# Kernel optimization log

Hardware: AMD Instinct MI355X
Metric: run time of the kernel (lower is better)

The kernel has to match this reference:

```python
import jax, jax.numpy as jnp
import numpy as np
from jax import lax

B, C, H, W = 8, 64, 256, 256
LENGTH = 9
REDUCTION = 8
HIDDEN = max(8, C // REDUCTION)


def _conv(x, w, b, pad):
    # x: [B,Cin,H,W], w: [Cout,Cin,kh,kw]
    y = lax.conv_general_dilated(x, w, (1, 1), [(pad, pad), (pad, pad)],
                                 dimension_numbers=('NCHW', 'OIHW', 'NCHW'))
    return y + b[None, :, None, None]


def _bilinear(img, cy, cx):
    # img: [B,C,H,W]; cy,cx: [B,H,W] float coords already clipped to [0, size-1]
    # Matches F.grid_sample(mode='bilinear', padding_mode='border', align_corners=True)
    Hh, Ww = img.shape[2], img.shape[3]
    y0 = jnp.floor(cy)
    x0 = jnp.floor(cx)
    wy = (cy - y0)[:, None]  # [B,1,H,W]
    wx = (cx - x0)[:, None]
    y0i = y0.astype(jnp.int32)
    x0i = x0.astype(jnp.int32)
    y1i = jnp.minimum(y0i + 1, Hh - 1)
    x1i = jnp.minimum(x0i + 1, Ww - 1)

    def g(im, iy, ix):
        return im[:, iy, ix]  # [C,H,W]

    gather = jax.vmap(g)
    v00 = gather(img, y0i, x0i)
    v01 = gather(img, y0i, x1i)
    v10 = gather(img, y1i, x0i)
    v11 = gather(img, y1i, x1i)
    return (v00 * (1 - wy) * (1 - wx) + v01 * (1 - wy) * wx
            + v10 * wy * (1 - wx) + v11 * wy * wx)


def _oriented_pool(x, vx, vy, length):
    # x: [B,C,H,W]; vx,vy: [B,1,H,W] direction fields
    _, _, Hh, Ww = x.shape
    yy = jnp.arange(Hh, dtype=x.dtype)[None, :, None]  # [1,H,1]
    xx = jnp.arange(Ww, dtype=x.dtype)[None, None, :]  # [1,1,W]
    half = length // 2
    offsets = jnp.arange(-half, half + 1, dtype=x.dtype)
    vx2 = vx[:, 0]  # [B,H,W]
    vy2 = vy[:, 0]

    def step(acc, t):
        cy = jnp.clip(yy + t * vy2, 0.0, Hh - 1)
        cx = jnp.clip(xx + t * vx2, 0.0, Ww - 1)
        return acc + _bilinear(x, cy, cx), None

    acc, _ = lax.scan(step, jnp.zeros_like(x), offsets)
    return acc / length


def setup_inputs() -> dict:
    key = jax.random.key(0)
    ks = jax.random.split(key, 5)

    def he(k, shape, fan_in):
        return jax.random.normal(k, shape, jnp.float32) * np.float32(1.0 / np.sqrt(fan_in))

    return {
        'x': jax.random.normal(ks[0], (B, C, H, W), jnp.float32),
        'w3': he(ks[1], (HIDDEN, C, 3, 3), C * 9),
        'b3': jnp.zeros((HIDDEN,), jnp.float32),
        'w1': he(ks[2], (1, HIDDEN, 1, 1), HIDDEN),
        'b1': jnp.zeros((1,), jnp.float32),
        'wr': he(ks[3], (HIDDEN, 2 * C, 1, 1), 2 * C),
        'br': jnp.zeros((HIDDEN,), jnp.float32),
        'we': he(ks[4], (2 * C, HIDDEN, 1, 1), HIDDEN),
        'be': jnp.zeros((2 * C,), jnp.float32),
    }


def reference(x, w3, b3, w1, b1, wr, br, we, be):
    theta = jnp.pi * jax.nn.sigmoid(_conv(jax.nn.relu(_conv(x, w3, b3, 1)), w1, b1, 0))  # [B,1,H,W]
    cos_t = jnp.cos(theta)
    sin_t = jnp.sin(theta)
    tan_feat = _oriented_pool(x, cos_t, sin_t, LENGTH)
    nor_feat = _oriented_pool(x, -sin_t, cos_t, LENGTH)
    context = jnp.concatenate([tan_feat, nor_feat], axis=1)  # [B,2C,H,W]
    w = jax.nn.sigmoid(_conv(jax.nn.relu(_conv(context, wr, br, 0)), we, be, 0))  # [B,2C,H,W]
    alpha_tan, alpha_norm = jnp.split(w, 2, axis=1)
    return (alpha_tan + alpha_norm) * x
```

## Files before the change

kernel.cpp:

```cpp
#include <hip/hip_runtime.h>
#include <math.h>

#define Bb 8
#define Cc 64
#define Hh 256
#define Ww 256
#define HID 8
#define PLANE (Hh*Ww)

#define T2H 6
#define T2W 66
#define T2P 67
#define T2N (T2H*T2W)

__global__ __launch_bounds__(256, 4) void theta_kernel(
    const float* __restrict__ x, const float* __restrict__ w3,
    const float* __restrict__ b3, const float* __restrict__ w1,
    const float* __restrict__ b1, float* __restrict__ cosout,
    float* __restrict__ sinout)
{
    __shared__ float2 tile[T2H * T2P];
    const int tid = threadIdx.x;
    const int tx = tid & 63;
    const int ty = tid >> 6;
    const int xx = blockIdx.x * 64 + tx;
    const int yy = blockIdx.y * 4 + ty;
    const int b  = blockIdx.z;
    const int row0 = blockIdx.y * 4 - 1;
    const int col0 = blockIdx.x * 64 - 1;

    const float* xb = x + (size_t)b * Cc * PLANE;

    int goff[2], loff[2];
    bool intile[2], inimg[2];
    #pragma unroll
    for (int k = 0; k < 2; k++) {
        const int i  = tid + k * 256;
        const int r  = i / T2W;
        const int cc = i - r * T2W;
        const int gy = row0 + r;
        const int gx = col0 + cc;
        intile[k] = (i < T2N);
        inimg[k]  = intile[k] && gy >= 0 && gy < Hh && gx >= 0 && gx < Ww;
        goff[k] = inimg[k] ? (gy * Ww + gx) : 0;
        loff[k] = r * T2P + cc;
    }

    float acc[HID];
    #pragma unroll
    for (int h = 0; h < HID; h++) acc[h] = 0.f;

    float rvx[2] = {0.f, 0.f}, rvy[2] = {0.f, 0.f};
    #pragma unroll
    for (int k = 0; k < 2; k++) if (inimg[k]) {
        rvx[k] = xb[goff[k]];
        rvy[k] = xb[goff[k] + PLANE];
    }

    const int lbase = (ty + 1) * T2P + (tx + 1);

    for (int cp = 0; cp < Cc / 2; cp++) {
        __syncthreads();
        #pragma unroll
        for (int k = 0; k < 2; k++)
            if (intile[k]) tile[loff[k]] = make_float2(rvx[k], rvy[k]);
        if (cp + 1 < Cc / 2) {
            const float* xn = xb + (size_t)(2 * (cp + 1)) * PLANE;
            #pragma unroll
            for (int k = 0; k < 2; k++) if (inimg[k]) {
                rvx[k] = xn[goff[k]];
                rvy[k] = xn[goff[k] + PLANE];
            }
        }
        __syncthreads();

        float2 v[9];
        #pragma unroll
        for (int dy = 0; dy < 3; dy++)
            #pragma unroll
            for (int dx = 0; dx < 3; dx++)
                v[dy * 3 + dx] = tile[lbase + (dy - 1) * T2P + (dx - 1)];

        #pragma unroll
        for (int h = 0; h < HID; h++) {
            const float* wk = w3 + (size_t)(h * Cc + 2 * cp) * 9;
            float a = acc[h];
            #pragma unroll
            for (int k = 0; k < 9; k++) a = fmaf(wk[k],     v[k].x, a);
            #pragma unroll
            for (int k = 0; k < 9; k++) a = fmaf(wk[9 + k], v[k].y, a);
            acc[h] = a;
        }
    }

    float z = b1[0];
    #pragma unroll
    for (int h = 0; h < HID; h++) {
        float hr = acc[h] + b3[h];
        hr = hr > 0.f ? hr : 0.f;
        z = fmaf(w1[h], hr, z);
    }
    const float theta = 3.14159265358979f / (1.f + __expf(-z));
    float s, co;
    __sincosf(theta, &s, &co);
    const int p = b * PLANE + yy * Ww + xx;
    cosout[p] = co;
    sinout[p] = s;
}

#define TPH 13
#define TPW 74
#define TPP 75
#define TPN (TPH*TPW)

__global__ __launch_bounds__(256, 3) void pool_kernel(
    const float* __restrict__ x,
    const float* __restrict__ cosb, const float* __restrict__ sinb,
    const float* __restrict__ wr, const float* __restrict__ br,
    const float* __restrict__ we, const float* __restrict__ be,
    float* __restrict__ out)
{
    __shared__ float2 tile[TPH * TPP];
    const int tid = threadIdx.x;
    const int tx = tid & 63;
    const int ty = tid >> 6;
    const int xx = blockIdx.x * 64 + tx;
    const int yy = blockIdx.y * 4 + ty;
    const int b  = blockIdx.z;
    const int p  = b * PLANE + yy * Ww + xx;
    const int row0 = blockIdx.y * 4 - 4;
    const int col0 = blockIdx.x * 64 - 4;

    const float vx = cosb[p];
    const float vy = sinb[p];

    int   off[16];
    float fwy[16], fwx[16];
    #pragma unroll
    for (int s = 0; s < 9; s++) {
        if (s == 4) continue;
        const int j = (s < 4) ? s : s - 1;
        const float t = (float)(s - 4);
        float cy = fminf(fmaxf((float)yy + t * vy, 0.f), (float)(Hh - 1));
        float cx = fminf(fmaxf((float)xx + t * vx, 0.f), (float)(Ww - 1));
        int y0 = min((int)cy, Hh - 2);
        int x0 = min((int)cx, Ww - 2);
        off[j] = (y0 - row0) * TPP + (x0 - col0);
        fwy[j] = cy - (float)y0;
        fwx[j] = cx - (float)x0;
        float cy2 = fminf(fmaxf((float)yy + t * vx, 0.f), (float)(Hh - 1));
        float cx2 = fminf(fmaxf((float)xx - t * vy, 0.f), (float)(Ww - 1));
        int y02 = min((int)cy2, Hh - 2);
        int x02 = min((int)cx2, Ww - 2);
        off[8 + j] = (y02 - row0) * TPP + (x02 - col0);
        fwy[8 + j] = cy2 - (float)y02;
        fwx[8 + j] = cx2 - (float)x02;
    }
    const int lcen = (ty + 4) * TPP + (tx + 4);

    int goff[4], loff[4];
    #pragma unroll
    for (int k = 0; k < 4; k++) {
        int i = tid + k * 256;
        i = (i < TPN) ? i : (TPN - 1);
        const int r  = i / TPW;
        const int cc = i - r * TPW;
        const int gy = min(max(row0 + r, 0), Hh - 1);
        const int gx = min(max(col0 + cc, 0), Ww - 1);
        goff[k] = gy * Ww + gx;
        loff[k] = r * TPP + cc;
    }

    float hid[HID];
    #pragma unroll
    for (int h = 0; h < HID; h++) hid[h] = br[h];

    const float* xb = x + (size_t)b * Cc * PLANE;

    float rvx[4], rvy[4];
    #pragma unroll
    for (int k = 0; k < 4; k++) {
        rvx[k] = xb[goff[k]];
        rvy[k] = xb[goff[k] + PLANE];
    }

    for (int cp = 0; cp < Cc / 2; cp++) {
        __syncthreads();
        #pragma unroll
        for (int k = 0; k < 4; k++)
            tile[loff[k]] = make_float2(rvx[k], rvy[k]);
        if (cp + 1 < Cc / 2) {
            const float* xn = xb + (size_t)(2 * (cp + 1)) * PLANE;
            #pragma unroll
            for (int k = 0; k < 4; k++) {
                rvx[k] = xn[goff[k]];
                rvy[k] = xn[goff[k] + PLANE];
            }
        }
        __syncthreads();

        const float2 cent = tile[lcen];
        float tacc0 = cent.x, tacc1 = cent.y;
        float nacc0 = cent.x, nacc1 = cent.y;
        #pragma unroll
        for (int s = 0; s < 16; s++) {
            const int o = off[s];
            const float2 a00 = tile[o];
            const float2 a01 = tile[o + 1];
            const float2 a10 = tile[o + TPP];
            const float2 a11 = tile[o + TPP + 1];
            const float wx_ = fwx[s], wy_ = fwy[s];
            const float t0  = a00.x + wx_ * (a01.x - a00.x);
            const float b0  = a10.x + wx_ * (a11.x - a10.x);
            const float v0  = t0 + wy_ * (b0 - t0);
            const float t1  = a00.y + wx_ * (a01.y - a00.y);
            const float b1v = a10.y + wx_ * (a11.y - a10.y);
            const float v1  = t1 + wy_ * (b1v - t1);
            if (s < 8) { tacc0 += v0; tacc1 += v1; }
            else       { nacc0 += v0; nacc1 += v1; }
        }
        tacc0 *= (1.f / 9.f); tacc1 *= (1.f / 9.f);
        nacc0 *= (1.f / 9.f); nacc1 *= (1.f / 9.f);
        const int c = 2 * cp;
        #pragma unroll
        for (int h = 0; h < HID; h++) {
            float a = hid[h];
            a = fmaf(wr[h * 128 + c],          tacc0, a);
            a = fmaf(wr[h * 128 + 64 + c],     nacc0, a);
            a = fmaf(wr[h * 128 + c + 1],      tacc1, a);
            a = fmaf(wr[h * 128 + 64 + c + 1], nacc1, a);
            hid[h] = a;
        }
    }

    #pragma unroll
    for (int h = 0; h < HID; h++) hid[h] = fmaxf(hid[h], 0.f);

    const int pix = yy * Ww + xx;
    for (int c = 0; c < Cc; c++) {
        float z1 = be[c];
        float z2 = be[c + 64];
        #pragma unroll
        for (int h = 0; h < HID; h++) {
            z1 = fmaf(we[c * 8 + h],        hid[h], z1);
            z2 = fmaf(we[(c + 64) * 8 + h], hid[h], z2);
        }
        const float a1 = 1.f / (1.f + __expf(-z1));
        const float a2 = 1.f / (1.f + __expf(-z2));
        const float xv = xb[c * PLANE + pix];
        out[(size_t)(b * Cc + c) * PLANE + pix] = (a1 + a2) * xv;
    }
}

extern "C" void kernel_launch(void* const* d_in, const int* in_sizes, int n_in,
                              void* d_out, int out_size, void* d_ws, size_t ws_size,
                              hipStream_t stream) {
    const float* x  = (const float*)d_in[0];
    const float* w3 = (const float*)d_in[1];
    const float* b3 = (const float*)d_in[2];
    const float* w1 = (const float*)d_in[3];
    const float* b1 = (const float*)d_in[4];
    const float* wr = (const float*)d_in[5];
    const float* br = (const float*)d_in[6];
    const float* we = (const float*)d_in[7];
    const float* be = (const float*)d_in[8];
    float* out = (float*)d_out;

    float* cosb = (float*)d_ws;
    float* sinb = cosb + (size_t)Bb * PLANE;

    dim3 grid(Ww / 64, Hh / 4, Bb);
    dim3 block(256);
    theta_kernel<<<grid, block, 0, stream>>>(x, w3, b3, w1, b1, cosb, sinb);
    pool_kernel<<<grid, block, 0, stream>>>(x, cosb, sinb, wr, br, we, be, out);
}
```

Before: 572.1 us.

## Stage more channels per LDS tile pass in theta and pool kernels

The theta kernel now stages 8 channels per iteration in two float4 shared tiles instead of 2 channels in a float2 tile. The pool kernel stages 4 channels per iteration in a float4 tile. Both changes cut the number of barrier-separated iterations and give wider LDS reads, while each bilinear offset and weight now serves more channels. Empty inline asm pins the offsets and weights in VGPRs so they are not rematerialized. The cost is higher register and LDS use (the pool tile doubles and the theta tiles quadruple), which may lower occupancy under the existing launch bounds.

After: 530.6 us. 7.3% less time.

```diff
diff --git a/kernel.cpp b/kernel.cpp
--- a/kernel.cpp
+++ b/kernel.cpp
@@ -8,6 +8,8 @@
 #define HID 8
 #define PLANE (Hh*Ww)
 
+typedef float fvec4 __attribute__((ext_vector_type(4)));
+
 #define T2H 6
 #define T2W 66
 #define T2P 67
@@ -19,7 +21,8 @@
     const float* __restrict__ b1, float* __restrict__ cosout,
     float* __restrict__ sinout)
 {
-    __shared__ float2 tile[T2H * T2P];
+    __shared__ fvec4 tileA[T2H * T2P];
+    __shared__ fvec4 tileB[T2H * T2P];
     const int tid = threadIdx.x;
     const int tx = tid & 63;
     const int ty = tid >> 6;
@@ -50,45 +53,60 @@
     #pragma unroll
     for (int h = 0; h < HID; h++) acc[h] = 0.f;
 
-    float rvx[2] = {0.f, 0.f}, rvy[2] = {0.f, 0.f};
+    float rv[2][8];
+    #pragma unroll
+    for (int k = 0; k < 2; k++)
+        #pragma unroll
+        for (int q = 0; q < 8; q++) rv[k][q] = 0.f;
     #pragma unroll
     for (int k = 0; k < 2; k++) if (inimg[k]) {
-        rvx[k] = xb[goff[k]];
-        rvy[k] = xb[goff[k] + PLANE];
+        #pragma unroll
+        for (int q = 0; q < 8; q++) rv[k][q] = xb[goff[k] + (size_t)q * PLANE];
     }
 
     const int lbase = (ty + 1) * T2P + (tx + 1);
 
-    for (int cp = 0; cp < Cc / 2; cp++) {
+    for (int st = 0; st < Cc / 8; st++) {
         __syncthreads();
         #pragma unroll
-        for (int k = 0; k < 2; k++)
-            if (intile[k]) tile[loff[k]] = make_float2(rvx[k], rvy[k]);
-        if (cp + 1 < Cc / 2) {
-            const float* xn = xb + (size_t)(2 * (cp + 1)) * PLANE;
+        for (int k = 0; k < 2; k++) if (intile[k]) {
+            tileA[loff[k]] = (fvec4){rv[k][0], rv[k][1], rv[k][2], rv[k][3]};
+            tileB[loff[k]] = (fvec4){rv[k][4], rv[k][5], rv[k][6], rv[k][7]};
+        }
+        if (st + 1 < Cc / 8) {
+            const float* xn = xb + (size_t)(st + 1) * 8 * PLANE;
             #pragma unroll
             for (int k = 0; k < 2; k++) if (inimg[k]) {
-                rvx[k] = xn[goff[k]];
-                rvy[k] = xn[goff[k] + PLANE];
+                #pragma unroll
+                for (int q = 0; q < 8; q++)
+                    rv[k][q] = xn[goff[k] + (size_t)q * PLANE];
             }
         }
         __syncthreads();
 
-        float2 v[9];
+        fvec4 va[9], vb[9];
         #pragma unroll
         for (int dy = 0; dy < 3; dy++)
             #pragma unroll
-            for (int dx = 0; dx < 3; dx++)
-                v[dy * 3 + dx] = tile[lbase + (dy - 1) * T2P + (dx - 1)];
+            for (int dx = 0; dx < 3; dx++) {
+                va[dy * 3 + dx] = tileA[lbase + (dy - 1) * T2P + (dx - 1)];
+                vb[dy * 3 + dx] = tileB[lbase + (dy - 1) * T2P + (dx - 1)];
+            }
 
         #pragma unroll
         for (int h = 0; h < HID; h++) {
-            const float* wk = w3 + (size_t)(h * Cc + 2 * cp) * 9;
+            const float* wk = w3 + (size_t)(h * Cc + st * 8) * 9;
             float a = acc[h];
             #pragma unroll
-            for (int k = 0; k < 9; k++) a = fmaf(wk[k],     v[k].x, a);
-            #pragma unroll
-            for (int k = 0; k < 9; k++) a = fmaf(wk[9 + k], v[k].y, a);
+            for (int c = 0; c < 4; c++)
+                #pragma unroll
+                for (int k = 0; k < 9; k++)
+                    a = fmaf(wk[c * 9 + k], va[k][c], a);
+            #pragma unroll
+            for (int c = 0; c < 4; c++)
+                #pragma unroll
+                for (int k = 0; k < 9; k++)
+                    a = fmaf(wk[(4 + c) * 9 + k], vb[k][c], a);
             acc[h] = a;
         }
     }
@@ -120,7 +138,7 @@
     const float* __restrict__ we, const float* __restrict__ be,
     float* __restrict__ out)
 {
-    __shared__ float2 tile[TPH * TPP];
+    __shared__ fvec4 tile[TPH * TPP];
     const int tid = threadIdx.x;
     const int tx = tid & 63;
     const int ty = tid >> 6;
@@ -156,6 +174,10 @@
         fwy[8 + j] = cy2 - (float)y02;
         fwx[8 + j] = cx2 - (float)x02;
     }
+    #pragma unroll
+    for (int s = 0; s < 16; s++)
+        asm volatile("" : "+v"(off[s]), "+v"(fwx[s]), "+v"(fwy[s]));
+
     const int lcen = (ty + 4) * TPP + (tx + 4);
 
     int goff[4], loff[4];
@@ -170,6 +192,9 @@
         goff[k] = gy * Ww + gx;
         loff[k] = r * TPP + cc;
     }
+    #pragma unroll
+    for (int k = 0; k < 4; k++)
+        asm volatile("" : "+v"(goff[k]), "+v"(loff[k]));
 
     float hid[HID];
     #pragma unroll
@@ -177,59 +202,61 @@
 
     const float* xb = x + (size_t)b * Cc * PLANE;
 
-    float rvx[4], rvy[4];
-    #pragma unroll
-    for (int k = 0; k < 4; k++) {
-        rvx[k] = xb[goff[k]];
-        rvy[k] = xb[goff[k] + PLANE];
-    }
-
-    for (int cp = 0; cp < Cc / 2; cp++) {
+    float rv[4][4];
+    #pragma unroll
+    for (int k = 0; k < 4; k++)
+        #pragma unroll
+        for (int q = 0; q < 4; q++)
+            rv[k][q] = xb[goff[k] + (size_t)q * PLANE];
+
+    for (int cp = 0; cp < Cc / 4; cp++) {
         __syncthreads();
         #pragma unroll
         for (int k = 0; k < 4; k++)
-            tile[loff[k]] = make_float2(rvx[k], rvy[k]);
-        if (cp + 1 < Cc / 2) {
-            const float* xn = xb + (size_t)(2 * (cp + 1)) * PLANE;
-            #pragma unroll
-            for (int k = 0; k < 4; k++) {
-                rvx[k] = xn[goff[k]];
-                rvy[k] = xn[goff[k] + PLANE];
-            }
+            tile[loff[k]] = (fvec4){rv[k][0], rv[k][1], rv[k][2], rv[k][3]};
+        if (cp + 1 < Cc / 4) {
+            const float* xn = xb + (size_t)(cp + 1) * 4 * PLANE;
+            #pragma unroll
+            for (int k = 0; k < 4; k++)
+                #pragma unroll
+                for (int q = 0; q < 4; q++)
+                    rv[k][q] = xn[goff[k] + (size_t)q * PLANE];
         }
         __syncthreads();
 
-        const float2 cent = tile[lcen];
-        float tacc0 = cent.x, tacc1 = cent.y;
-        float nacc0 = cent.x, nacc1 = cent.y;
+        const fvec4 cent = tile[lcen];
+        float tac[4], nac[4];
+        #pragma unroll
+        for (int q = 0; q < 4; q++) { tac[q] = cent[q]; nac[q] = cent[q]; }
+
         #pragma unroll
         for (int s = 0; s < 16; s++) {
             const int o = off[s];
-            const float2 a00 = tile[o];
-            const float2 a01 = tile[o + 1];
-            const float2 a10 = tile[o + TPP];
-            const float2 a11 = tile[o + TPP + 1];
+            const fvec4 a00 = tile[o];
+            const fvec4 a01 = tile[o + 1];
+            const fvec4 a10 = tile[o + TPP];
+            const fvec4 a11 = tile[o + TPP + 1];
             const float wx_ = fwx[s], wy_ = fwy[s];
-            const float t0  = a00.x + wx_ * (a01.x - a00.x);
-            const float b0  = a10.x + wx_ * (a11.x - a10.x);
-            const float v0  = t0 + wy_ * (b0 - t0);
-            const float t1  = a00.y + wx_ * (a01.y - a00.y);
-            const float b1v = a10.y + wx_ * (a11.y - a10.y);
-            const float v1  = t1 + wy_ * (b1v - t1);
-            if (s < 8) { tacc0 += v0; tacc1 += v1; }
-            else       { nacc0 += v0; nacc1 += v1; }
-        }
-        tacc0 *= (1.f / 9.f); tacc1 *= (1.f / 9.f);
-        nacc0 *= (1.f / 9.f); nacc1 *= (1.f / 9.f);
-        const int c = 2 * cp;
-        #pragma unroll
-        for (int h = 0; h < HID; h++) {
-            float a = hid[h];
-            a = fmaf(wr[h * 128 + c],          tacc0, a);
-            a = fmaf(wr[h * 128 + 64 + c],     nacc0, a);
-            a = fmaf(wr[h * 128 + c + 1],      tacc1, a);
-            a = fmaf(wr[h * 128 + 64 + c + 1], nacc1, a);
-            hid[h] = a;
+            #pragma unroll
+            for (int q = 0; q < 4; q++) {
+                const float tq = a00[q] + wx_ * (a01[q] - a00[q]);
+                const float bq = a10[q] + wx_ * (a11[q] - a10[q]);
+                const float vq = tq + wy_ * (bq - tq);
+                if (s < 8) tac[q] += vq; else nac[q] += vq;
+            }
+        }
+        const int c = 4 * cp;
+        #pragma unroll
+        for (int q = 0; q < 4; q++) {
+            const float tq = tac[q] * (1.f / 9.f);
+            const float nq = nac[q] * (1.f / 9.f);
+            #pragma unroll
+            for (int h = 0; h < HID; h++) {
+                float a = hid[h];
+                a = fmaf(wr[h * 128 + c + q],      tq, a);
+                a = fmaf(wr[h * 128 + 64 + c + q], nq, a);
+                hid[h] = a;
+            }
         }
     }
 
```
